# Performance work log

Hardware: AMD Instinct MI355X
Metric: run time of the kernel (lower is better)

## Reference

```python
import jax, jax.numpy as jnp
import numpy as np

B, H, T, D = 2, 16, 2048, 64


def setup_inputs() -> dict:
    key = jax.random.key(0)
    kq, kk, kv, km = jax.random.split(key, 4)
    q = jax.random.normal(kq, (B, H, T, D), dtype=jnp.float32)
    k = jax.random.normal(kk, (B, H, T, D), dtype=jnp.float32)
    v = jax.random.normal(kv, (B, H, T, D), dtype=jnp.float32)
    mask = jax.random.randint(km, (T, T), 0, 2, dtype=jnp.int32)
    return {"q": q, "k": k, "v": v, "mask": mask}


def reference(q, k, v, mask):
    d_k = q.shape[-1]
    scale = jnp.asarray(d_k, q.dtype) ** -0.5
    # (B,H,T,D) @ (B,H,D,T) -> (B,H,T,T)
    scores = jnp.einsum("bhtd,bhsd->bhts", q * scale, k)
    # mask broadcast over (B,H); masked positions set to -1e9 as in torch code
    scores = jnp.where(mask[None, None, :, :] == 0, jnp.asarray(-1e9, scores.dtype), scores)
    attn = jax.nn.softmax(scores, axis=-1)
    # (B,H,T,T) @ (B,H,T,D) -> (B,H,T,D)
    out = jnp.einsum("bhts,bhsd->bhtd", attn, v)
    return (out, attn)
```

## Files before the change

### kernel.cpp

```cpp
#include <hip/hip_runtime.h>
#include <hip/hip_bf16.h>
#include <cstddef>

#define T_SEQ 2048
#define D_HEAD 64
#define BC 64
#define NKT (T_SEQ / BC)
#define PAD 72

typedef __bf16 bf16x8 __attribute__((ext_vector_type(8)));
typedef float f32x4 __attribute__((ext_vector_type(4)));
typedef unsigned short u16x8 __attribute__((ext_vector_type(8)));

__device__ __forceinline__ unsigned short f2bf(float f) {
  __bf16 h = (__bf16)f;
  return __builtin_bit_cast(unsigned short, h);
}
__device__ __forceinline__ bf16x8 ldfrag(const unsigned short* p) {
  u16x8 t = *(const u16x8*)p;
  return __builtin_bit_cast(bf16x8, t);
}
__device__ __forceinline__ f32x4 mfma16(bf16x8 a, bf16x8 b, f32x4 c) {
  return __builtin_amdgcn_mfma_f32_16x16x32_bf16(a, b, c, 0, 0, 0);
}
__device__ __forceinline__ void bar_sync() {
  asm volatile("" ::: "memory");
  __builtin_amdgcn_s_barrier();
  asm volatile("" ::: "memory");
}
__device__ __forceinline__ void lds_fence() {
  asm volatile("s_waitcnt lgkmcnt(0)" ::: "memory");
}
__device__ __forceinline__ float exp2_hw(float x) { return __builtin_amdgcn_exp2f(x); }
__device__ __forceinline__ float log2_hw(float x) { return __builtin_amdgcn_logf(x); }

__global__ __launch_bounds__(256) void mask_pack(const int* __restrict__ maskg,
                                                 unsigned* __restrict__ mp) {
  const size_t total = (size_t)T_SEQ * T_SEQ;
  size_t idx = (size_t)blockIdx.x * blockDim.x + threadIdx.x;
  const size_t stride = (size_t)gridDim.x * blockDim.x;
  const int lane = threadIdx.x & 63;
  for (; idx < total; idx += stride) {
    int mv = maskg[idx];
    unsigned long long b = __ballot(mv != 0);
    if (lane == 0)       mp[idx >> 5] = (unsigned)b;
    else if (lane == 32) mp[idx >> 5] = (unsigned)(b >> 32);
  }
}

__global__ __launch_bounds__(256, 5) void attn_fused2(
    const float* __restrict__ qg, const float* __restrict__ kg,
    const float* __restrict__ vg, const unsigned* __restrict__ mpk,
    float* __restrict__ outg, float* __restrict__ attng)
{
  __shared__ unsigned short ks[BC][PAD];
  __shared__ unsigned short vt[D_HEAD][PAD];
  __shared__ unsigned short ps[64][PAD];

  const int bid = blockIdx.x;
  const int lin = (bid & 7) * 128 + (bid >> 3);
  const int bh  = lin >> 5;
  const int strip = lin & 31;

  const int tid  = threadIdx.x;
  const int lane = tid & 63;
  const int wid  = tid >> 6;
  const int lr = lane & 15, lh = lane >> 4;
  const int r0 = strip * 64 + wid * 16;
  const int sv = tid >> 2;
  const int sc4 = (tid & 3) << 4;

  const float C = 0.18033688011112042f;
  const float* qb = qg + (size_t)bh * T_SEQ * D_HEAD;
  const float* kb = kg + (size_t)bh * T_SEQ * D_HEAD;
  const float* vb = vg + (size_t)bh * T_SEQ * D_HEAD;
  const int ROWW = T_SEQ / 32;

  bf16x8 qf[2];
  {
    const float* qr = qb + (size_t)(r0 + lr) * D_HEAD;
    #pragma unroll
    for (int kk = 0; kk < 2; ++kk) {
      float4 a = *(const float4*)(qr + kk * 32 + lh * 8);
      float4 b = *(const float4*)(qr + kk * 32 + lh * 8 + 4);
      u16x8 u;
      u[0] = f2bf(a.x); u[1] = f2bf(a.y); u[2] = f2bf(a.z); u[3] = f2bf(a.w);
      u[4] = f2bf(b.x); u[5] = f2bf(b.y); u[6] = f2bf(b.z); u[7] = f2bf(b.w);
      qf[kk] = __builtin_bit_cast(bf16x8, u);
    }
  }

  const f32x4 zero4 = {0.f, 0.f, 0.f, 0.f};
  f32x4 acc[4];
  #pragma unroll
  for (int nt = 0; nt < 4; ++nt) acc[nt] = zero4;
  float psum[4] = {0.f, 0.f, 0.f, 0.f};

  for (int kt = 0; kt < NKT; ++kt) {
    const int n0 = kt * BC;
    bar_sync();
    {
      const float* ksrc = kb + (size_t)(n0 + sv) * D_HEAD + sc4;
      const float* vsrc = vb + (size_t)(n0 + sv) * D_HEAD + sc4;
      float4 k0 = *(const float4*)(ksrc + 0),  k1 = *(const float4*)(ksrc + 4);
      float4 k2 = *(const float4*)(ksrc + 8),  k3 = *(const float4*)(ksrc + 12);
      float4 v0 = *(const float4*)(vsrc + 0),  v1 = *(const float4*)(vsrc + 4);
      float4 v2 = *(const float4*)(vsrc + 8),  v3 = *(const float4*)(vsrc + 12);
      *(ushort4*)&ks[sv][sc4 + 0]  = make_ushort4(f2bf(k0.x), f2bf(k0.y), f2bf(k0.z), f2bf(k0.w));
      *(ushort4*)&ks[sv][sc4 + 4]  = make_ushort4(f2bf(k1.x), f2bf(k1.y), f2bf(k1.z), f2bf(k1.w));
      *(ushort4*)&ks[sv][sc4 + 8]  = make_ushort4(f2bf(k2.x), f2bf(k2.y), f2bf(k2.z), f2bf(k2.w));
      *(ushort4*)&ks[sv][sc4 + 12] = make_ushort4(f2bf(k3.x), f2bf(k3.y), f2bf(k3.z), f2bf(k3.w));
      vt[sc4 + 0 ][sv] = f2bf(v0.x); vt[sc4 + 1 ][sv] = f2bf(v0.y);
      vt[sc4 + 2 ][sv] = f2bf(v0.z); vt[sc4 + 3 ][sv] = f2bf(v0.w);
      vt[sc4 + 4 ][sv] = f2bf(v1.x); vt[sc4 + 5 ][sv] = f2bf(v1.y);
      vt[sc4 + 6 ][sv] = f2bf(v1.z); vt[sc4 + 7 ][sv] = f2bf(v1.w);
      vt[sc4 + 8 ][sv] = f2bf(v2.x); vt[sc4 + 9 ][sv] = f2bf(v2.y);
      vt[sc4 + 10][sv] = f2bf(v2.z); vt[sc4 + 11][sv] = f2bf(v2.w);
      vt[sc4 + 12][sv] = f2bf(v3.x); vt[sc4 + 13][sv] = f2bf(v3.y);
      vt[sc4 + 14][sv] = f2bf(v3.z); vt[sc4 + 15][sv] = f2bf(v3.w);
    }
    unsigned mw[4][2];
    #pragma unroll
    for (int r = 0; r < 4; ++r) {
      const size_t mrow = (size_t)(r0 + 4 * lh + r) * ROWW + kt * 2;
      mw[r][0] = mpk[mrow];
      mw[r][1] = mpk[mrow + 1];
    }
    lds_fence(); bar_sync();

    f32x4 sc_[4];
    #pragma unroll
    for (int nt = 0; nt < 4; ++nt) sc_[nt] = zero4;
    #pragma unroll
    for (int kk = 0; kk < 2; ++kk) {
      bf16x8 kf[4];
      #pragma unroll
      for (int nt = 0; nt < 4; ++nt) kf[nt] = ldfrag(&ks[nt * 16 + lr][kk * 32 + lh * 8]);
      #pragma unroll
      for (int nt = 0; nt < 4; ++nt) sc_[nt] = mfma16(qf[kk], kf[nt], sc_[nt]);
    }
    #pragma unroll
    for (int r = 0; r < 4; ++r) {
      #pragma unroll
      for (int nt = 0; nt < 4; ++nt) {
        const int mv = (mw[r][nt >> 1] >> ((nt & 1) * 16 + lr)) & 1;
        const float p = mv ? exp2_hw(sc_[nt][r] * C) : 0.f;
        psum[r] += p;
        ps[wid * 16 + 4 * lh + r][nt * 16 + lr] = f2bf(p);
      }
    }
    lds_fence();
    #pragma unroll
    for (int kk = 0; kk < 2; ++kk) {
      const bf16x8 pa = ldfrag(&ps[wid * 16 + lr][kk * 32 + lh * 8]);
      #pragma unroll
      for (int nt = 0; nt < 4; ++nt) {
        const bf16x8 vf = ldfrag(&vt[nt * 16 + lr][kk * 32 + lh * 8]);
        acc[nt] = mfma16(pa, vf, acc[nt]);
      }
    }
  }

  float iv[4], lg2iv[4];
  #pragma unroll
  for (int r = 0; r < 4; ++r) {
    float s = psum[r];
    s += __shfl_xor(s, 1);
    s += __shfl_xor(s, 2);
    s += __shfl_xor(s, 4);
    s += __shfl_xor(s, 8);
    iv[r] = 1.0f / s;
    lg2iv[r] = log2_hw(iv[r]);
  }

  float* ob = outg + (size_t)(bh * T_SEQ + r0) * D_HEAD;
  #pragma unroll
  for (int nt = 0; nt < 4; ++nt)
    #pragma unroll
    for (int r = 0; r < 4; ++r)
      ob[(size_t)(4 * lh + r) * D_HEAD + nt * 16 + lr] = acc[nt][r] * iv[r];

  float* ab = attng + (size_t)(bh * T_SEQ + r0) * T_SEQ;
  for (int kt = 0; kt < NKT; ++kt) {
    const int n0 = kt * BC;
    bar_sync();
    {
      const float* ksrc = kb + (size_t)(n0 + sv) * D_HEAD + sc4;
      float4 k0 = *(const float4*)(ksrc + 0),  k1 = *(const float4*)(ksrc + 4);
      float4 k2 = *(const float4*)(ksrc + 8),  k3 = *(const float4*)(ksrc + 12);
      *(ushort4*)&ks[sv][sc4 + 0]  = make_ushort4(f2bf(k0.x), f2bf(k0.y), f2bf(k0.z), f2bf(k0.w));
      *(ushort4*)&ks[sv][sc4 + 4]  = make_ushort4(f2bf(k1.x), f2bf(k1.y), f2bf(k1.z), f2bf(k1.w));
      *(ushort4*)&ks[sv][sc4 + 8]  = make_ushort4(f2bf(k2.x), f2bf(k2.y), f2bf(k2.z), f2bf(k2.w));
      *(ushort4*)&ks[sv][sc4 + 12] = make_ushort4(f2bf(k3.x), f2bf(k3.y), f2bf(k3.z), f2bf(k3.w));
    }
    unsigned mw[4][2];
    #pragma unroll
    for (int r = 0; r < 4; ++r) {
      const size_t mrow = (size_t)(r0 + 4 * lh + r) * ROWW + kt * 2;
      mw[r][0] = mpk[mrow];
      mw[r][1] = mpk[mrow + 1];
    }
    lds_fence(); bar_sync();

    f32x4 sc_[4];
    #pragma unroll
    for (int nt = 0; nt < 4; ++nt) sc_[nt] = zero4;
    #pragma unroll
    for (int kk = 0; kk < 2; ++kk) {
      bf16x8 kf[4];
      #pragma unroll
      for (int nt = 0; nt < 4; ++nt) kf[nt] = ldfrag(&ks[nt * 16 + lr][kk * 32 + lh * 8]);
      #pragma unroll
      for (int nt = 0; nt < 4; ++nt) sc_[nt] = mfma16(qf[kk], kf[nt], sc_[nt]);
    }
    #pragma unroll
    for (int r = 0; r < 4; ++r) {
      float* arow = ab + (size_t)(4 * lh + r) * T_SEQ + n0;
      #pragma unroll
      for (int nt = 0; nt < 4; ++nt) {
        const int mv = (mw[r][nt >> 1] >> ((nt & 1) * 16 + lr)) & 1;
        const float p = mv ? exp2_hw(__builtin_fmaf(sc_[nt][r], C, lg2iv[r])) : 0.f;
        __builtin_nontemporal_store(p, arow + nt * 16 + lr);
      }
    }
  }
}

__global__ __launch_bounds__(512, 2) void attn_fused_fb(
    const float* __restrict__ qg, const float* __restrict__ kg,
    const float* __restrict__ vg, const int* __restrict__ maskg,
    float* __restrict__ outg, float* __restrict__ attng)
{
  __shared__ unsigned short qs[128][PAD];
  __shared__ unsigned short ks[64][PAD];
  __shared__ unsigned short vt[64][PAD];
  __shared__ unsigned short pp[128][PAD];
  __shared__ float rsum[128];
  int bid = blockIdx.x;
  int lin = (bid & 7) * 64 + (bid >> 3);
  int bh = lin >> 4, br0 = (lin & 15) * 128;
  const int tid = threadIdx.x, lane = tid & 63, wid = tid >> 6;
  const int wm = wid >> 1, wn = wid & 1, lr = lane & 15, lh = lane >> 4;
  const float scale = 0.125f;
  const float* qb = qg + ((size_t)bh * T_SEQ + br0) * D_HEAD;
  const float* kbp = kg + (size_t)bh * T_SEQ * D_HEAD;
  const float* vbp = vg + (size_t)bh * T_SEQ * D_HEAD;
  if (tid < 128) rsum[tid] = 0.f;
  #pragma unroll
  for (int it = 0; it < 4; ++it) {
    int idx = it * 512 + tid;
    int r = idx >> 4, c = (idx & 15) << 2;
    float4 f = *(const float4*)(qb + (size_t)r * D_HEAD + c);
    *(ushort4*)&qs[r][c] = make_ushort4(f2bf(f.x), f2bf(f.y), f2bf(f.z), f2bf(f.w));
  }
  f32x4 acc_o[2][2];
  const f32x4 zero4 = {0.f, 0.f, 0.f, 0.f};
  #pragma unroll
  for (int a = 0; a < 2; ++a)
    #pragma unroll
    for (int b = 0; b < 2; ++b) acc_o[a][b] = zero4;
  float psum[2][4] = {{0.f,0.f,0.f,0.f},{0.f,0.f,0.f,0.f}};
  __syncthreads();
  for (int kt = 0; kt < NKT; ++kt) {
    const int kb0 = kt * 64;
    #pragma unroll
    for (int it = 0; it < 2; ++it) {
      int idx = it * 512 + tid;
      int r = idx >> 4, c = (idx & 15) << 2;
      float4 f = *(const float4*)(kbp + (size_t)(kb0 + r) * D_HEAD + c);
      *(ushort4*)&ks[r][c] = make_ushort4(f2bf(f.x), f2bf(f.y), f2bf(f.z), f2bf(f.w));
      float4 g = *(const float4*)(vbp + (size_t)(kb0 + r) * D_HEAD + c);
      vt[c+0][r] = f2bf(g.x); vt[c+1][r] = f2bf(g.y);
      vt[c+2][r] = f2bf(g.z); vt[c+3][r] = f2bf(g.w);
    }
    __syncthreads();
    f32x4 sc[2][2];
    #pragma unroll
    for (int a = 0; a < 2; ++a)
      #pragma unroll
      for (int b = 0; b < 2; ++b) sc[a][b] = zero4;
    #pragma unroll
    for (int kk = 0; kk < 2; ++kk) {
      const int ke = kk * 32 + lh * 8;
      bf16x8 af[2], bfq[2];
      #pragma unroll
      for (int mt = 0; mt < 2; ++mt) af[mt] = ldfrag(&qs[wm*32 + mt*16 + lr][ke]);
      #pragma unroll
      for (int nt = 0; nt < 2; ++nt) bfq[nt] = ldfrag(&ks[wn*32 + nt*16 + lr][ke]);
      #pragma unroll
      for (int mt = 0; mt < 2; ++mt)
        #pragma unroll
        for (int nt = 0; nt < 2; ++nt)
          sc[mt][nt] = mfma16(af[mt], bfq[nt], sc[mt][nt]);
    }
    #pragma unroll
    for (int mt = 0; mt < 2; ++mt)
      #pragma unroll
      for (int nt = 0; nt < 2; ++nt)
        #pragma unroll
        for (int r = 0; r < 4; ++r) {
          int row = wm*32 + mt*16 + lh*4 + r, col = wn*32 + nt*16 + lr;
          int mv = maskg[(size_t)(br0 + row) * T_SEQ + (kb0 + col)];
          float p = mv ? __expf(sc[mt][nt][r] * scale) : 0.f;
          psum[mt][r] += p;
          pp[row][col] = f2bf(p);
        }
    __syncthreads();
    #pragma unroll
    for (int kk = 0; kk < 2; ++kk) {
      const int ke = kk * 32 + lh * 8;
      bf16x8 pa[2], vf[2];
      #pragma unroll
      for (int mt = 0; mt < 2; ++mt) pa[mt] = ldfrag(&pp[wm*32 + mt*16 + lr][ke]);
      #pragma unroll
      for (int nt = 0; nt < 2; ++nt) vf[nt] = ldfrag(&vt[wn*32 + nt*16 + lr][ke]);
      #pragma unroll
      for (int mt = 0; mt < 2; ++mt)
        #pragma unroll
        for (int nt = 0; nt < 2; ++nt)
          acc_o[mt][nt] = mfma16(pa[mt], vf[nt], acc_o[mt][nt]);
    }
    __syncthreads();
  }
  #pragma unroll
  for (int mt = 0; mt < 2; ++mt)
    #pragma unroll
    for (int r = 0; r < 4; ++r) {
      float sv = psum[mt][r];
      sv += __shfl_xor(sv, 1); sv += __shfl_xor(sv, 2);
      sv += __shfl_xor(sv, 4); sv += __shfl_xor(sv, 8);
      if (lr == 0) atomicAdd(&rsum[wm*32 + mt*16 + lh*4 + r], sv);
    }
  __syncthreads();
  float invs[2][4];
  #pragma unroll
  for (int mt = 0; mt < 2; ++mt)
    #pragma unroll
    for (int r = 0; r < 4; ++r)
      invs[mt][r] = 1.0f / rsum[wm*32 + mt*16 + lh*4 + r];
  float* ob = outg + ((size_t)bh * T_SEQ + br0) * D_HEAD;
  #pragma unroll
  for (int mt = 0; mt < 2; ++mt)
    #pragma unroll
    for (int nt = 0; nt < 2; ++nt)
      #pragma unroll
      for (int r = 0; r < 4; ++r) {
        int row = wm*32 + mt*16 + lh*4 + r, col = wn*32 + nt*16 + lr;
        ob[(size_t)row * D_HEAD + col] = acc_o[mt][nt][r] * invs[mt][r];
      }
  float* ab = attng + (size_t)bh * T_SEQ * T_SEQ + (size_t)br0 * T_SEQ;
  for (int kt = 0; kt < NKT; ++kt) {
    const int kb0 = kt * 64;
    __syncthreads();
    #pragma unroll
    for (int it = 0; it < 2; ++it) {
      int idx = it * 512 + tid;
      int r = idx >> 4, c = (idx & 15) << 2;
      float4 f = *(const float4*)(kbp + (size_t)(kb0 + r) * D_HEAD + c);
      *(ushort4*)&ks[r][c] = make_ushort4(f2bf(f.x), f2bf(f.y), f2bf(f.z), f2bf(f.w));
    }
    __syncthreads();
    f32x4 sc[2][2];
    #pragma unroll
    for (int a = 0; a < 2; ++a)
      #pragma unroll
      for (int b = 0; b < 2; ++b) sc[a][b] = zero4;
    #pragma unroll
    for (int kk = 0; kk < 2; ++kk) {
      const int ke = kk * 32 + lh * 8;
      bf16x8 af[2], bfq[2];
      #pragma unroll
      for (int mt = 0; mt < 2; ++mt) af[mt] = ldfrag(&qs[wm*32 + mt*16 + lr][ke]);
      #pragma unroll
      for (int nt = 0; nt < 2; ++nt) bfq[nt] = ldfrag(&ks[wn*32 + nt*16 + lr][ke]);
      #pragma unroll
      for (int mt = 0; mt < 2; ++mt)
        #pragma unroll
        for (int nt = 0; nt < 2; ++nt)
          sc[mt][nt] = mfma16(af[mt], bfq[nt], sc[mt][nt]);
    }
    #pragma unroll
    for (int mt = 0; mt < 2; ++mt)
      #pragma unroll
      for (int nt = 0; nt < 2; ++nt)
        #pragma unroll
        for (int r = 0; r < 4; ++r) {
          int row = wm*32 + mt*16 + lh*4 + r, col = wn*32 + nt*16 + lr;
          int mv = maskg[(size_t)(br0 + row) * T_SEQ + (kb0 + col)];
          float p = mv ? __expf(sc[mt][nt][r] * scale) * invs[mt][r] : 0.f;
          ab[(size_t)row * T_SEQ + kb0 + col] = p;
        }
  }
}

extern "C" void kernel_launch(void* const* d_in, const int* in_sizes, int n_in,
                              void* d_out, int out_size, void* d_ws, size_t ws_size,
                              hipStream_t stream) {
  const float* q = (const float*)d_in[0];
  const float* k = (const float*)d_in[1];
  const float* v = (const float*)d_in[2];
  const int* mask = (const int*)d_in[3];
  float* out = (float*)d_out;
  float* attn = out + (size_t)2 * 16 * T_SEQ * D_HEAD;

  const size_t mpk_bytes = (size_t)T_SEQ * T_SEQ / 8;
  if (ws_size >= mpk_bytes) {
    unsigned* mp = (unsigned*)d_ws;
    mask_pack<<<dim3(2048), 256, 0, stream>>>(mask, mp);
    attn_fused2<<<dim3(1024), 256, 0, stream>>>(q, k, v, mp, out, attn);
  } else {
    attn_fused_fb<<<dim3(512), 512, 0, stream>>>(q, k, v, mask, out, attn);
  }
}
```

Before: 209.3 us.

## Transpose QK^T MFMA to write P rows packed; restructure V transpose loads

The first pass now computes S^T by swapping the MFMA operands, so each lane holds four consecutive key columns of one query row. P can then be written to LDS as packed 32-bit pairs, the row sum becomes a single per-lane scalar, and only one mask word pair is loaded per lane. The V tile is loaded with a new thread mapping (two rows by strided columns) so each thread writes packed bf16 pairs into the transposed LDS tile instead of sixteen scalar 16-bit stores. The aim is fewer LDS store instructions and fewer bank conflicts, at the cost of extra cross-lane shuffles to redistribute the inverse row sums and less coalesced scalar global loads for V.

```diff
diff --git a/kernel.cpp b/kernel.cpp
--- a/kernel.cpp
+++ b/kernel.cpp
@@ -69,6 +69,8 @@
   const int r0 = strip * 64 + wid * 16;
   const int sv = tid >> 2;
   const int sc4 = (tid & 3) << 4;
+  const int vt7 = tid & 7;
+  const int vs2 = (tid >> 3) * 2;
 
   const float C = 0.18033688011112042f;
   const float* qb = qg + (size_t)bh * T_SEQ * D_HEAD;
@@ -94,60 +96,60 @@
   f32x4 acc[4];
   #pragma unroll
   for (int nt = 0; nt < 4; ++nt) acc[nt] = zero4;
-  float psum[4] = {0.f, 0.f, 0.f, 0.f};
+  float psum_s = 0.f;
 
   for (int kt = 0; kt < NKT; ++kt) {
     const int n0 = kt * BC;
     bar_sync();
     {
       const float* ksrc = kb + (size_t)(n0 + sv) * D_HEAD + sc4;
-      const float* vsrc = vb + (size_t)(n0 + sv) * D_HEAD + sc4;
       float4 k0 = *(const float4*)(ksrc + 0),  k1 = *(const float4*)(ksrc + 4);
       float4 k2 = *(const float4*)(ksrc + 8),  k3 = *(const float4*)(ksrc + 12);
-      float4 v0 = *(const float4*)(vsrc + 0),  v1 = *(const float4*)(vsrc + 4);
-      float4 v2 = *(const float4*)(vsrc + 8),  v3 = *(const float4*)(vsrc + 12);
       *(ushort4*)&ks[sv][sc4 + 0]  = make_ushort4(f2bf(k0.x), f2bf(k0.y), f2bf(k0.z), f2bf(k0.w));
       *(ushort4*)&ks[sv][sc4 + 4]  = make_ushort4(f2bf(k1.x), f2bf(k1.y), f2bf(k1.z), f2bf(k1.w));
       *(ushort4*)&ks[sv][sc4 + 8]  = make_ushort4(f2bf(k2.x), f2bf(k2.y), f2bf(k2.z), f2bf(k2.w));
       *(ushort4*)&ks[sv][sc4 + 12] = make_ushort4(f2bf(k3.x), f2bf(k3.y), f2bf(k3.z), f2bf(k3.w));
-      vt[sc4 + 0 ][sv] = f2bf(v0.x); vt[sc4 + 1 ][sv] = f2bf(v0.y);
-      vt[sc4 + 2 ][sv] = f2bf(v0.z); vt[sc4 + 3 ][sv] = f2bf(v0.w);
-      vt[sc4 + 4 ][sv] = f2bf(v1.x); vt[sc4 + 5 ][sv] = f2bf(v1.y);
-      vt[sc4 + 6 ][sv] = f2bf(v1.z); vt[sc4 + 7 ][sv] = f2bf(v1.w);
-      vt[sc4 + 8 ][sv] = f2bf(v2.x); vt[sc4 + 9 ][sv] = f2bf(v2.y);
-      vt[sc4 + 10][sv] = f2bf(v2.z); vt[sc4 + 11][sv] = f2bf(v2.w);
-      vt[sc4 + 12][sv] = f2bf(v3.x); vt[sc4 + 13][sv] = f2bf(v3.y);
-      vt[sc4 + 14][sv] = f2bf(v3.z); vt[sc4 + 15][sv] = f2bf(v3.w);
-    }
-    unsigned mw[4][2];
-    #pragma unroll
-    for (int r = 0; r < 4; ++r) {
-      const size_t mrow = (size_t)(r0 + 4 * lh + r) * ROWW + kt * 2;
-      mw[r][0] = mpk[mrow];
-      mw[r][1] = mpk[mrow + 1];
-    }
+    }
+    {
+      const float* v0 = vb + (size_t)(n0 + vs2) * D_HEAD + vt7;
+      const float* v1 = v0 + D_HEAD;
+      #pragma unroll
+      for (int j = 0; j < 8; ++j) {
+        const float a = v0[8 * j];
+        const float b = v1[8 * j];
+        const unsigned w = (unsigned)f2bf(a) | ((unsigned)f2bf(b) << 16);
+        *(unsigned*)&vt[vt7 + 8 * j][vs2] = w;
+      }
+    }
+    const unsigned mw0 = mpk[(size_t)(r0 + lr) * ROWW + kt * 2];
+    const unsigned mw1 = mpk[(size_t)(r0 + lr) * ROWW + kt * 2 + 1];
     lds_fence(); bar_sync();
 
-    f32x4 sc_[4];
-    #pragma unroll
-    for (int nt = 0; nt < 4; ++nt) sc_[nt] = zero4;
+    f32x4 st[4];
+    #pragma unroll
+    for (int nt = 0; nt < 4; ++nt) st[nt] = zero4;
     #pragma unroll
     for (int kk = 0; kk < 2; ++kk) {
       bf16x8 kf[4];
       #pragma unroll
       for (int nt = 0; nt < 4; ++nt) kf[nt] = ldfrag(&ks[nt * 16 + lr][kk * 32 + lh * 8]);
       #pragma unroll
-      for (int nt = 0; nt < 4; ++nt) sc_[nt] = mfma16(qf[kk], kf[nt], sc_[nt]);
-    }
-    #pragma unroll
-    for (int r = 0; r < 4; ++r) {
-      #pragma unroll
-      for (int nt = 0; nt < 4; ++nt) {
-        const int mv = (mw[r][nt >> 1] >> ((nt & 1) * 16 + lr)) & 1;
-        const float p = mv ? exp2_hw(sc_[nt][r] * C) : 0.f;
-        psum[r] += p;
-        ps[wid * 16 + 4 * lh + r][nt * 16 + lr] = f2bf(p);
+      for (int nt = 0; nt < 4; ++nt) st[nt] = mfma16(kf[nt], qf[kk], st[nt]);
+    }
+    #pragma unroll
+    for (int nt = 0; nt < 4; ++nt) {
+      const unsigned w = (nt & 2) ? mw1 : mw0;
+      float p[4];
+      #pragma unroll
+      for (int r = 0; r < 4; ++r) {
+        const int bit = (nt & 1) * 16 + 4 * lh + r;
+        p[r] = ((w >> bit) & 1) ? exp2_hw(st[nt][r] * C) : 0.f;
+        psum_s += p[r];
       }
+      const unsigned w0 = (unsigned)f2bf(p[0]) | ((unsigned)f2bf(p[1]) << 16);
+      const unsigned w1 = (unsigned)f2bf(p[2]) | ((unsigned)f2bf(p[3]) << 16);
+      *(unsigned*)&ps[wid * 16 + lr][nt * 16 + 4 * lh]     = w0;
+      *(unsigned*)&ps[wid * 16 + lr][nt * 16 + 4 * lh + 2] = w1;
     }
     lds_fence();
     #pragma unroll
@@ -161,16 +163,16 @@
     }
   }
 
-  float iv[4], lg2iv[4];
+  {
+    psum_s += __shfl_xor(psum_s, 16);
+    psum_s += __shfl_xor(psum_s, 32);
+  }
+  const float iv_s = 1.0f / psum_s;
+  float ivq[4], lg2ivq[4];
   #pragma unroll
   for (int r = 0; r < 4; ++r) {
-    float s = psum[r];
-    s += __shfl_xor(s, 1);
-    s += __shfl_xor(s, 2);
-    s += __shfl_xor(s, 4);
-    s += __shfl_xor(s, 8);
-    iv[r] = 1.0f / s;
-    lg2iv[r] = log2_hw(iv[r]);
+    ivq[r] = __shfl(iv_s, 4 * lh + r);
+    lg2ivq[r] = log2_hw(ivq[r]);
   }
 
   float* ob = outg + (size_t)(bh * T_SEQ + r0) * D_HEAD;
@@ -178,7 +180,7 @@
   for (int nt = 0; nt < 4; ++nt)
     #pragma unroll
     for (int r = 0; r < 4; ++r)
-      ob[(size_t)(4 * lh + r) * D_HEAD + nt * 16 + lr] = acc[nt][r] * iv[r];
+      ob[(size_t)(4 * lh + r) * D_HEAD + nt * 16 + lr] = acc[nt][r] * ivq[r];
 
   float* ab = attng + (size_t)(bh * T_SEQ + r0) * T_SEQ;
   for (int kt = 0; kt < NKT; ++kt) {
@@ -219,7 +221,7 @@
       #pragma unroll
       for (int nt = 0; nt < 4; ++nt) {
         const int mv = (mw[r][nt >> 1] >> ((nt & 1) * 16 + lr)) & 1;
-        const float p = mv ? exp2_hw(__builtin_fmaf(sc_[nt][r], C, lg2iv[r])) : 0.f;
+        const float p = mv ? exp2_hw(__builtin_fmaf(sc_[nt][r], C, lg2ivq[r])) : 0.f;
         __builtin_nontemporal_store(p, arow + nt * 16 + lr);
       }
     }
```

Measured after the change: 190.4 us. 9.0% less time.
